# Performance work log

Hardware: AMD Instinct MI355X
Metric: run time of the kernel (lower is better)

Reference implementation:

```python
import jax, jax.numpy as jnp
import numpy as np

CODEC_RANGE = 1.0
COMMIT_WEIGHT = 0.1


def setup_inputs() -> dict:
    key = jax.random.key(0)
    ks = jax.random.split(key, 6)
    B, T, D, Dc, NQ, BINS = 8, 4096, 512, 256, 8, 1024
    return {
        "x": jax.random.normal(ks[0], (B, T, D), dtype=jnp.float32),
        "in_w": jax.random.normal(ks[1], (Dc, D), dtype=jnp.float32) * (1.0 / np.sqrt(D)),
        "in_b": jnp.zeros((Dc,), dtype=jnp.float32),
        "out_w": jax.random.normal(ks[2], (D, Dc), dtype=jnp.float32) * (1.0 / np.sqrt(Dc)),
        "out_b": jnp.zeros((D,), dtype=jnp.float32),
        "codebooks": jax.random.normal(ks[3], (NQ, BINS, Dc), dtype=jnp.float32),
    }


def reference(x, in_w, in_b, out_w, out_b, codebooks):
    # input projection + tanh range limiting
    h = jnp.tanh(x @ in_w.T + in_b) * CODEC_RANGE  # [B, T, Dc]

    def step(residual, codebook):
        # squared L2 distances: ||r||^2 - 2 r.e + ||e||^2  -> [B, T, bins]
        r2 = jnp.sum(residual * residual, axis=-1, keepdims=True)
        e2 = jnp.sum(codebook * codebook, axis=-1)  # [bins]
        dist = r2 - 2.0 * jnp.einsum("btd,nd->btn", residual, codebook) + e2
        idx = jnp.argmin(dist, axis=-1)  # [B, T]
        q = codebook[idx]  # gather -> [B, T, Dc]
        # commitment loss vs. detached quantized vectors
        commit = jnp.mean((jax.lax.stop_gradient(q) - residual) ** 2)
        return residual - q, (q, idx, commit)

    _, (qs, idxs, commits) = jax.lax.scan(step, h, codebooks)
    quantized = jnp.sum(qs, axis=0)  # [B, T, Dc]
    # straight-through estimator
    quantized = h + jax.lax.stop_gradient(quantized - h)
    out = quantized @ out_w.T + out_b  # [B, T, D]
    commit_loss = COMMIT_WEIGHT * jnp.sum(commits)
    return out, idxs, commit_loss
```

## Files before the change

kernel.cpp:

```cpp
#include <hip/hip_runtime.h>
#include <math.h>

#define DC 256
#define NBINS 1024
#define NQ 8
#define NTOK 32768
#define D_IN 512
#define DCH 32
#define TOK 64
#define STG_BLOCKS (NTOK / TOK)
#define MARGIN 5e-3f

typedef __attribute__((ext_vector_type(8))) short short8v;
typedef __attribute__((ext_vector_type(4))) float f32x4;

__device__ __forceinline__ unsigned short f2bf(float x) {
  unsigned u = __float_as_uint(x);
  return (unsigned short)((u + 0x7fffu + ((u >> 16) & 1u)) >> 16);
}
__device__ __forceinline__ float bf2f(unsigned short h) {
  return __uint_as_float(((unsigned)h) << 16);
}
__device__ __forceinline__ void store8s(unsigned short* dst, const unsigned short* v) {
  uint4 u;
  u.x = v[0] | ((unsigned)v[1] << 16); u.y = v[2] | ((unsigned)v[3] << 16);
  u.z = v[4] | ((unsigned)v[5] << 16); u.w = v[6] | ((unsigned)v[7] << 16);
  *reinterpret_cast<uint4*>(dst) = u;
}
__device__ __forceinline__ short8v load8s(const unsigned short* p) {
  return __builtin_bit_cast(short8v, *reinterpret_cast<const float4*>(p));
}

__device__ __forceinline__ float np_sumsq128(const float* a) {
#pragma clang fp contract(off)
  float r0 = a[0] * a[0], r1 = a[1] * a[1], r2 = a[2] * a[2], r3 = a[3] * a[3];
  float r4 = a[4] * a[4], r5 = a[5] * a[5], r6 = a[6] * a[6], r7 = a[7] * a[7];
  for (int i = 8; i < 128; i += 8) {
    r0 += a[i + 0] * a[i + 0]; r1 += a[i + 1] * a[i + 1];
    r2 += a[i + 2] * a[i + 2]; r3 += a[i + 3] * a[i + 3];
    r4 += a[i + 4] * a[i + 4]; r5 += a[i + 5] * a[i + 5];
    r6 += a[i + 6] * a[i + 6]; r7 += a[i + 7] * a[i + 7];
  }
  return ((r0 + r1) + (r2 + r3)) + ((r4 + r5) + (r6 + r7));
}
__device__ __forceinline__ float np_sumsq256(const float* a) {
#pragma clang fp contract(off)
  float lo = np_sumsq128(a);
  float hi = np_sumsq128(a + 128);
  return lo + hi;
}

__global__ void e2_np_kernel(const float* __restrict__ cb, float* __restrict__ e2) {
  int b = blockIdx.x * 256 + threadIdx.x;
  e2[b] = np_sumsq256(cb + (size_t)b * DC);
}

__global__ void presplit_kernel(const float* __restrict__ cb,
                                unsigned short* __restrict__ cb_h,
                                unsigned short* __restrict__ cb_l) {
  int id = blockIdx.x * 256 + threadIdx.x;
  int sk = id >> 10, bin = id & 1023;
  int s = sk >> 5, k8 = sk & 31;
  const float* src = cb + ((size_t)s * NBINS + bin) * DC + k8 * 8;
  unsigned short hh[8], ll[8];
#pragma unroll
  for (int j = 0; j < 8; ++j) {
    float x = src[j];
    unsigned short h = f2bf(x);
    hh[j] = h;
    ll[j] = f2bf(x - bf2f(h));
  }
  store8s(cb_h + (size_t)id * 8, hh);
  store8s(cb_l + (size_t)id * 8, ll);
}

__global__ __launch_bounds__(256) void in_proj_kernel(
    const float* __restrict__ x, const float* __restrict__ in_w,
    const float* __restrict__ in_b, float* __restrict__ res) {
  __shared__ __align__(16) float aT[DCH][68];
  __shared__ __align__(16) float bT[DCH][68];
  const int thr = threadIdx.x;
  const int tx = thr & 15, ty = thr >> 4;
  const int m0 = blockIdx.x * 64, n0 = blockIdx.y * 64;
  float acc[4][4] = {};
  float s1[4][4] = {};
  for (int kc = 0; kc < D_IN; kc += DCH) {
    if (kc == 384) {
#pragma unroll
      for (int i = 0; i < 4; ++i)
#pragma unroll
        for (int j = 0; j < 4; ++j) { s1[i][j] = acc[i][j]; acc[i][j] = 0.f; }
    }
    __syncthreads();
#pragma unroll
    for (int i = 0; i < 2; ++i) {
      int q = thr + 256 * i;
      int m = q >> 3, kk = (q & 7) << 2;
      float4 v = *reinterpret_cast<const float4*>(x + (size_t)(m0 + m) * D_IN + kc + kk);
      aT[kk + 0][m] = v.x; aT[kk + 1][m] = v.y; aT[kk + 2][m] = v.z; aT[kk + 3][m] = v.w;
      float4 w = *reinterpret_cast<const float4*>(in_w + (size_t)(n0 + m) * D_IN + kc + kk);
      bT[kk + 0][m] = w.x; bT[kk + 1][m] = w.y; bT[kk + 2][m] = w.z; bT[kk + 3][m] = w.w;
    }
    __syncthreads();
#pragma unroll 8
    for (int d = 0; d < DCH; ++d) {
      float4 a = *reinterpret_cast<const float4*>(&aT[d][ty * 4]);
      float4 b = *reinterpret_cast<const float4*>(&bT[d][tx * 4]);
      float av[4] = {a.x, a.y, a.z, a.w};
      float bv[4] = {b.x, b.y, b.z, b.w};
#pragma unroll
      for (int i = 0; i < 4; ++i)
#pragma unroll
        for (int j = 0; j < 4; ++j) acc[i][j] = fmaf(av[i], bv[j], acc[i][j]);
    }
  }
#pragma unroll
  for (int i = 0; i < 4; ++i) {
    int m = m0 + ty * 4 + i, n = n0 + tx * 4;
    float4 hv;
#pragma unroll
    for (int j = 0; j < 4; ++j) {
#pragma clang fp contract(off)
      float c = s1[i][j] + acc[i][j];
      float pre = c + in_b[n + j];
      ((float*)&hv)[j] = tanhf(pre);
    }
    *reinterpret_cast<float4*>(res + (size_t)m * DC + n) = hv;
  }
}

__global__ __launch_bounds__(256, 2) void score_kernel(
    const float* __restrict__ e2,
    const unsigned short* __restrict__ cb_h, const unsigned short* __restrict__ cb_l,
    const float* __restrict__ res, int* __restrict__ win_g, int* __restrict__ flag_g,
    int s) {
  __shared__ __align__(16) unsigned short a_hi[32 * TOK * 8];
  __shared__ __align__(16) unsigned short a_lo[32 * TOK * 8];
  __shared__ float m1s[4 * TOK], m2s[4 * TOK];
  __shared__ int   i1s[4 * TOK];

  const int thr = threadIdx.x;
  const int lane = thr & 63;
  const int w = thr >> 6;
  const int lg = lane >> 4;
  const int lc = lane & 15;
  const int m0 = blockIdx.x * TOK;
  const float* e2s = e2 + (size_t)s * NBINS;
  const unsigned short* bhp = cb_h + (size_t)s * (32 * 1024 * 8);
  const unsigned short* blp = cb_l + (size_t)s * (32 * 1024 * 8);

  {
    int row = thr >> 2, d0 = (thr & 3) << 6;
    const float* rrow = res + (size_t)(m0 + row) * DC + d0;
#pragma unroll
    for (int c = 0; c < 8; ++c) {
      float4 r0 = *reinterpret_cast<const float4*>(rrow + c * 8);
      float4 r1 = *reinterpret_cast<const float4*>(rrow + c * 8 + 4);
      float rv[8] = {r0.x, r0.y, r0.z, r0.w, r1.x, r1.y, r1.z, r1.w};
      unsigned short hh[8], ll[8];
#pragma unroll
      for (int j = 0; j < 8; ++j) {
        float xv = -2.0f * rv[j];
        unsigned short h = f2bf(xv);
        hh[j] = h; ll[j] = f2bf(xv - bf2f(h));
      }
      int k8 = (d0 >> 3) + c;
      store8s(a_hi + ((size_t)k8 * TOK + row) * 8, hh);
      store8s(a_lo + ((size_t)k8 * TOK + row) * 8, ll);
    }
  }
  m1s[thr] = 3.4028235e38f; m2s[thr] = 3.4028235e38f; i1s[thr] = 0;
  __syncthreads();

  for (int c = 0; c < 4; ++c) {
    const int bbase = w * 256 + c * 64;
    f32x4 acc[4][4];
#pragma unroll
    for (int nt = 0; nt < 4; ++nt) {
      float ev = e2s[bbase + nt * 16 + lc];
      f32x4 iv = {ev, ev, ev, ev};
#pragma unroll
      for (int rt = 0; rt < 4; ++rt) acc[rt][nt] = iv;
    }
#pragma unroll 2
    for (int kstep = 0; kstep < 8; ++kstep) {
      short8v ah[4], al[4];
#pragma unroll
      for (int rt = 0; rt < 4; ++rt) {
        int off = ((kstep * 4 + lg) * TOK + rt * 16 + lc) * 8;
        ah[rt] = load8s(a_hi + off);
        al[rt] = load8s(a_lo + off);
      }
      short8v bh[4], bl[4];
#pragma unroll
      for (int nt = 0; nt < 4; ++nt) {
        size_t boff = ((size_t)(kstep * 4 + lg) * 1024 + bbase + nt * 16 + lc) * 8;
        bh[nt] = load8s(bhp + boff);
        bl[nt] = load8s(blp + boff);
      }
#pragma unroll
      for (int nt = 0; nt < 4; ++nt)
#pragma unroll
        for (int rt = 0; rt < 4; ++rt)
          acc[rt][nt] = __builtin_amdgcn_mfma_f32_16x16x32_bf16(ah[rt], bh[nt], acc[rt][nt], 0, 0, 0);
#pragma unroll
      for (int nt = 0; nt < 4; ++nt)
#pragma unroll
        for (int rt = 0; rt < 4; ++rt)
          acc[rt][nt] = __builtin_amdgcn_mfma_f32_16x16x32_bf16(ah[rt], bl[nt], acc[rt][nt], 0, 0, 0);
#pragma unroll
      for (int nt = 0; nt < 4; ++nt)
#pragma unroll
        for (int rt = 0; rt < 4; ++rt)
          acc[rt][nt] = __builtin_amdgcn_mfma_f32_16x16x32_bf16(al[rt], bh[nt], acc[rt][nt], 0, 0, 0);
    }
#pragma unroll
    for (int rt = 0; rt < 4; ++rt)
#pragma unroll
      for (int reg = 0; reg < 4; ++reg) {
        float m1 = 3.4028235e38f, m2 = 3.4028235e38f; int i1 = 0;
#pragma unroll
        for (int nt = 0; nt < 4; ++nt) {
          float v = acc[rt][nt][reg];
          int b = bbase + nt * 16 + lc;
          if (v < m1) { m2 = m1; m1 = v; i1 = b; }
          else m2 = fminf(m2, v);
        }
#pragma unroll
        for (int msk = 1; msk < 16; msk <<= 1) {
          float om1 = __shfl_xor(m1, msk, 64);
          float om2 = __shfl_xor(m2, msk, 64);
          int   oi1 = __shfl_xor(i1, msk, 64);
          if (om1 < m1 || (om1 == m1 && oi1 < i1)) { m2 = fminf(m1, om2); m1 = om1; i1 = oi1; }
          else m2 = fminf(m2, om1);
        }
        if (lc == 0) {
          int sidx = w * TOK + rt * 16 + lg * 4 + reg;
          float pm1 = m1s[sidx], pm2 = m2s[sidx]; int pi1 = i1s[sidx];
          if (m1 < pm1 || (m1 == pm1 && i1 < pi1)) {
            m1s[sidx] = m1; m2s[sidx] = fminf(pm1, m2); i1s[sidx] = i1;
          } else {
            m2s[sidx] = fminf(pm2, m1);
          }
        }
      }
  }
  __syncthreads();
  if (thr < TOK) {
    float m1 = m1s[thr], m2 = m2s[thr]; int i1 = i1s[thr];
#pragma unroll
    for (int ww = 1; ww < 4; ++ww) {
      float om1 = m1s[ww * TOK + thr], om2 = m2s[ww * TOK + thr];
      int oi1 = i1s[ww * TOK + thr];
      if (om1 < m1 || (om1 == m1 && oi1 < i1)) { m2 = fminf(m1, om2); m1 = om1; i1 = oi1; }
      else m2 = fminf(m2, om1);
    }
    win_g[m0 + thr] = i1;
    flag_g[m0 + thr] = (m2 - m1 < MARGIN) ? 1 : 0;
  }
}

__global__ __launch_bounds__(256) void fix_kernel(
    const float* __restrict__ cb, const float* __restrict__ e2,
    const int* __restrict__ win_g, const int* __restrict__ flag_g,
    float* __restrict__ res, float* __restrict__ idx_f, double* __restrict__ partial,
    int s) {
  __shared__ int win_l[TOK], flag_l[TOK];
  __shared__ __align__(16) float rrow_s[256];
  __shared__ float redf[4];
  __shared__ int   redi[4];
  __shared__ double wsum[4];
  const int thr = threadIdx.x;
  const int lane = thr & 63;
  const int w = thr >> 6;
  const int m0 = blockIdx.x * TOK;
  const float* cbs = cb + (size_t)s * NBINS * DC;
  const float* e2s = e2 + (size_t)s * NBINS;
  double sqacc = 0.0;

  if (thr < TOK) { win_l[thr] = win_g[m0 + thr]; flag_l[thr] = flag_g[m0 + thr]; }
  __syncthreads();
  for (int row = 0; row < TOK; ++row) {
    if (!flag_l[row]) continue;
    if (thr < 64)
      reinterpret_cast<float4*>(rrow_s)[thr] =
          reinterpret_cast<const float4*>(res + (size_t)(m0 + row) * DC)[thr];
    __syncthreads();
    float r2 = np_sumsq256(rrow_s);
    float best = 3.4028235e38f; int bb = 0;
#pragma unroll
    for (int jj = 0; jj < 4; ++jj) {
      int b = thr * 4 + jj;
      const float4* e4 = reinterpret_cast<const float4*>(cbs + (size_t)b * DC);
      const float4* r4 = reinterpret_cast<const float4*>(rrow_s);
      float accv = 0.f;
      for (int q = 0; q < 64; ++q) {
        float4 ev = e4[q], rv = r4[q];
        accv = fmaf(rv.x, ev.x, accv);
        accv = fmaf(rv.y, ev.y, accv);
        accv = fmaf(rv.z, ev.z, accv);
        accv = fmaf(rv.w, ev.w, accv);
      }
      {
#pragma clang fp contract(off)
        float t = r2 - 2.0f * accv;
        float dist = t + e2s[b];
        if (dist < best) { best = dist; bb = b; }
      }
    }
#pragma unroll
    for (int msk = 1; msk < 64; msk <<= 1) {
      float ov = __shfl_xor(best, msk, 64);
      int   ob = __shfl_xor(bb, msk, 64);
      if (ov < best || (ov == best && ob < bb)) { best = ov; bb = ob; }
    }
    if (lane == 0) { redf[w] = best; redi[w] = bb; }
    __syncthreads();
    if (thr == 0) {
      float bs = redf[0]; int bfin = redi[0];
#pragma unroll
      for (int ww = 1; ww < 4; ++ww)
        if (redf[ww] < bs || (redf[ww] == bs && redi[ww] < bfin)) { bs = redf[ww]; bfin = redi[ww]; }
      win_l[row] = bfin;
    }
    __syncthreads();
  }
  {
    int row = thr >> 2, d0 = (thr & 3) << 6;
    int wbin = win_l[row];
    const float* erow = cbs + (size_t)wbin * DC + d0;
    float* rrow = res + (size_t)(m0 + row) * DC + d0;
#pragma unroll
    for (int c = 0; c < 8; ++c) {
      float4 r0 = *reinterpret_cast<const float4*>(rrow + c * 8);
      float4 r1 = *reinterpret_cast<const float4*>(rrow + c * 8 + 4);
      float4 e0 = *reinterpret_cast<const float4*>(erow + c * 8);
      float4 e1 = *reinterpret_cast<const float4*>(erow + c * 8 + 4);
      float nv[8] = {r0.x - e0.x, r0.y - e0.y, r0.z - e0.z, r0.w - e0.w,
                     r1.x - e1.x, r1.y - e1.y, r1.z - e1.z, r1.w - e1.w};
#pragma unroll
      for (int j = 0; j < 8; ++j) sqacc += (double)nv[j] * nv[j];
      *reinterpret_cast<float4*>(rrow + c * 8) = (float4){nv[0], nv[1], nv[2], nv[3]};
      *reinterpret_cast<float4*>(rrow + c * 8 + 4) = (float4){nv[4], nv[5], nv[6], nv[7]};
    }
    if (thr < TOK) idx_f[(size_t)s * NTOK + m0 + thr] = (float)win_l[thr];
  }
#pragma unroll
  for (int msk = 1; msk < 64; msk <<= 1) sqacc += __shfl_xor(sqacc, msk, 64);
  if (lane == 0) wsum[w] = sqacc;
  __syncthreads();
  if (thr == 0) {
    double t = 0.0;
#pragma unroll
    for (int ww = 0; ww < 4; ++ww) t += wsum[ww];
    partial[(size_t)s * STG_BLOCKS + blockIdx.x] = t;
  }
}

__global__ void finalize_kernel(const double* __restrict__ partial, float* __restrict__ out_last) {
  __shared__ double acc_s[64];
  int t = threadIdx.x;
  double a = 0.0;
  for (int i = 0; i < 64; ++i) a += partial[(size_t)t * 64 + i];
  acc_s[t] = a;
  __syncthreads();
  if (t == 0) {
    double tot = 0.0;
    for (int i = 0; i < 64; ++i) tot += acc_s[i];
    out_last[0] = (float)(0.1 * tot / 8388608.0);
  }
}

__global__ __launch_bounds__(256) void out_proj_kernel(
    const float* __restrict__ cb, const float* __restrict__ idx_f,
    const float* __restrict__ out_w, const float* __restrict__ out_b,
    float* __restrict__ out) {
  __shared__ __align__(16) float aT[DCH][68];
  __shared__ __align__(16) float bT[DCH][68];
  __shared__ int idx_l[NQ][64];
  const int thr = threadIdx.x;
  const int tx = thr & 15, ty = thr >> 4;
  const int m0 = blockIdx.x * 64, n0 = blockIdx.y * 64;
#pragma unroll
  for (int i = 0; i < 2; ++i) {
    int q = thr + 256 * i;
    int s = q >> 6, m = q & 63;
    idx_l[s][m] = (int)idx_f[(size_t)s * NTOK + m0 + m];
  }
  float acc[4][4] = {};
  for (int kc = 0; kc < DC; kc += DCH) {
    __syncthreads();
#pragma unroll
    for (int i = 0; i < 2; ++i) {
      int q = thr + 256 * i;
      int m = q >> 3, kk = (q & 7) << 2;
      float4 v = {0.f, 0.f, 0.f, 0.f};
#pragma unroll
      for (int s = 0; s < NQ; ++s) {
        const float4 e = *reinterpret_cast<const float4*>(
            cb + ((size_t)s * NBINS + idx_l[s][m]) * DC + kc + kk);
        v.x += e.x; v.y += e.y; v.z += e.z; v.w += e.w;
      }
      aT[kk + 0][m] = v.x; aT[kk + 1][m] = v.y; aT[kk + 2][m] = v.z; aT[kk + 3][m] = v.w;
      float4 wv = *reinterpret_cast<const float4*>(out_w + (size_t)(n0 + m) * DC + kc + kk);
      bT[kk + 0][m] = wv.x; bT[kk + 1][m] = wv.y; bT[kk + 2][m] = wv.z; bT[kk + 3][m] = wv.w;
    }
    __syncthreads();
#pragma unroll 8
    for (int d = 0; d < DCH; ++d) {
      float4 a = *reinterpret_cast<const float4*>(&aT[d][ty * 4]);
      float4 b = *reinterpret_cast<const float4*>(&bT[d][tx * 4]);
      float av[4] = {a.x, a.y, a.z, a.w};
      float bv[4] = {b.x, b.y, b.z, b.w};
#pragma unroll
      for (int i = 0; i < 4; ++i)
#pragma unroll
        for (int j = 0; j < 4; ++j) acc[i][j] = fmaf(av[i], bv[j], acc[i][j]);
    }
  }
#pragma unroll
  for (int i = 0; i < 4; ++i) {
    int m = m0 + ty * 4 + i, n = n0 + tx * 4;
    float4 o;
    o.x = acc[i][0] + out_b[n + 0];
    o.y = acc[i][1] + out_b[n + 1];
    o.z = acc[i][2] + out_b[n + 2];
    o.w = acc[i][3] + out_b[n + 3];
    *reinterpret_cast<float4*>(out + (size_t)m * D_IN + n) = o;
  }
}

extern "C" void kernel_launch(void* const* d_in, const int* in_sizes, int n_in,
                              void* d_out, int out_size, void* d_ws, size_t ws_size,
                              hipStream_t stream) {
  (void)in_sizes; (void)n_in; (void)out_size; (void)d_ws; (void)ws_size;
  const float* x     = (const float*)d_in[0];
  const float* in_w  = (const float*)d_in[1];
  const float* in_b  = (const float*)d_in[2];
  const float* out_w = (const float*)d_in[3];
  const float* out_b = (const float*)d_in[4];
  const float* cb    = (const float*)d_in[5];
  float* out = (float*)d_out;
  float* res    = out;
  float* e2     = out + 8388608;
  double* part  = (double*)(out + 8404992);
  unsigned short* cb_h = (unsigned short*)(out + 9000000);
  unsigned short* cb_l = (unsigned short*)(out + 10500000);
  int* win_g   = (int*)(out + 11600000);
  int* flag_g  = (int*)(out + 11700000);
  float* idx_f  = out + 16777216;
  float* c_out  = out + 17039360;

  hipLaunchKernelGGL(e2_np_kernel, dim3(32), dim3(256), 0, stream, cb, e2);
  hipLaunchKernelGGL(presplit_kernel, dim3(1024), dim3(256), 0, stream, cb, cb_h, cb_l);
  hipLaunchKernelGGL(in_proj_kernel, dim3(512, 4), dim3(256), 0, stream, x, in_w, in_b, res);
  for (int s = 0; s < NQ; ++s) {
    hipLaunchKernelGGL(score_kernel, dim3(STG_BLOCKS), dim3(256), 0, stream,
                       e2, cb_h, cb_l, res, win_g, flag_g, s);
    hipLaunchKernelGGL(fix_kernel, dim3(STG_BLOCKS), dim3(256), 0, stream,
                       cb, e2, win_g, flag_g, res, idx_f, part, s);
  }
  hipLaunchKernelGGL(finalize_kernel, dim3(1), dim3(64), 0, stream, part, c_out);
  hipLaunchKernelGGL(out_proj_kernel, dim3(512, 8), dim3(256), 0, stream, cb, idx_f, out_w, out_b, out);
}
```

Before: 1.562 ms.

## Move output projection to bf16x3 MFMA with full-N tiles per block

The output projection now runs on MFMA bf16 instructions, using a hi/lo split (three products) to keep near-fp32 accuracy, in place of scalar FMA tiling. Each block handles 32 tokens across all 512 output columns. The summed codebook vectors are gathered once per token into shared memory, which removes the repeated gathers the old 64x64 tiling did for every N tile. out_w is read directly from global memory and split into bf16 halves inside the loop, which adds conversion ALU work and uncoalesced weight loads. Stores are scalar and strided.

```diff
diff --git a/kernel.cpp b/kernel.cpp
--- a/kernel.cpp
+++ b/kernel.cpp
@@ -26,6 +26,12 @@
   u.x = v[0] | ((unsigned)v[1] << 16); u.y = v[2] | ((unsigned)v[3] << 16);
   u.z = v[4] | ((unsigned)v[5] << 16); u.w = v[6] | ((unsigned)v[7] << 16);
   *reinterpret_cast<uint4*>(dst) = u;
+}
+__device__ __forceinline__ short8v pack8s(const unsigned short* v) {
+  uint4 u;
+  u.x = v[0] | ((unsigned)v[1] << 16); u.y = v[2] | ((unsigned)v[3] << 16);
+  u.z = v[4] | ((unsigned)v[5] << 16); u.w = v[6] | ((unsigned)v[7] << 16);
+  return __builtin_bit_cast(short8v, u);
 }
 __device__ __forceinline__ short8v load8s(const unsigned short* p) {
   return __builtin_bit_cast(short8v, *reinterpret_cast<const float4*>(p));
@@ -375,59 +381,95 @@
     const float* __restrict__ cb, const float* __restrict__ idx_f,
     const float* __restrict__ out_w, const float* __restrict__ out_b,
     float* __restrict__ out) {
-  __shared__ __align__(16) float aT[DCH][68];
-  __shared__ __align__(16) float bT[DCH][68];
-  __shared__ int idx_l[NQ][64];
+  __shared__ __align__(16) unsigned short a_hi[32 * 32 * 8];
+  __shared__ __align__(16) unsigned short a_lo[32 * 32 * 8];
   const int thr = threadIdx.x;
-  const int tx = thr & 15, ty = thr >> 4;
-  const int m0 = blockIdx.x * 64, n0 = blockIdx.y * 64;
-#pragma unroll
-  for (int i = 0; i < 2; ++i) {
-    int q = thr + 256 * i;
-    int s = q >> 6, m = q & 63;
-    idx_l[s][m] = (int)idx_f[(size_t)s * NTOK + m0 + m];
-  }
-  float acc[4][4] = {};
-  for (int kc = 0; kc < DC; kc += DCH) {
-    __syncthreads();
-#pragma unroll
-    for (int i = 0; i < 2; ++i) {
-      int q = thr + 256 * i;
-      int m = q >> 3, kk = (q & 7) << 2;
-      float4 v = {0.f, 0.f, 0.f, 0.f};
+  const int lane = thr & 63;
+  const int w = thr >> 6;
+  const int lg = lane >> 4;
+  const int lc = lane & 15;
+  const int m0 = blockIdx.x * 32;
+
+  {
+    int row = thr >> 3, d0 = (thr & 7) << 5;
+    int m = m0 + row;
+    int idxs[NQ];
+#pragma unroll
+    for (int s = 0; s < NQ; ++s) idxs[s] = (int)idx_f[(size_t)s * NTOK + m];
+#pragma unroll
+    for (int c = 0; c < 4; ++c) {
+      int d = d0 + c * 8;
+      float q[8] = {0.f, 0.f, 0.f, 0.f, 0.f, 0.f, 0.f, 0.f};
 #pragma unroll
       for (int s = 0; s < NQ; ++s) {
-        const float4 e = *reinterpret_cast<const float4*>(
-            cb + ((size_t)s * NBINS + idx_l[s][m]) * DC + kc + kk);
-        v.x += e.x; v.y += e.y; v.z += e.z; v.w += e.w;
-      }
-      aT[kk + 0][m] = v.x; aT[kk + 1][m] = v.y; aT[kk + 2][m] = v.z; aT[kk + 3][m] = v.w;
-      float4 wv = *reinterpret_cast<const float4*>(out_w + (size_t)(n0 + m) * DC + kc + kk);
-      bT[kk + 0][m] = wv.x; bT[kk + 1][m] = wv.y; bT[kk + 2][m] = wv.z; bT[kk + 3][m] = wv.w;
-    }
-    __syncthreads();
-#pragma unroll 8
-    for (int d = 0; d < DCH; ++d) {
-      float4 a = *reinterpret_cast<const float4*>(&aT[d][ty * 4]);
-      float4 b = *reinterpret_cast<const float4*>(&bT[d][tx * 4]);
-      float av[4] = {a.x, a.y, a.z, a.w};
-      float bv[4] = {b.x, b.y, b.z, b.w};
-#pragma unroll
-      for (int i = 0; i < 4; ++i)
-#pragma unroll
-        for (int j = 0; j < 4; ++j) acc[i][j] = fmaf(av[i], bv[j], acc[i][j]);
-    }
-  }
-#pragma unroll
-  for (int i = 0; i < 4; ++i) {
-    int m = m0 + ty * 4 + i, n = n0 + tx * 4;
-    float4 o;
-    o.x = acc[i][0] + out_b[n + 0];
-    o.y = acc[i][1] + out_b[n + 1];
-    o.z = acc[i][2] + out_b[n + 2];
-    o.w = acc[i][3] + out_b[n + 3];
-    *reinterpret_cast<float4*>(out + (size_t)m * D_IN + n) = o;
-  }
+        const float4* e4 = reinterpret_cast<const float4*>(
+            cb + ((size_t)s * NBINS + idxs[s]) * DC + d);
+        float4 e0 = e4[0], e1 = e4[1];
+        q[0] += e0.x; q[1] += e0.y; q[2] += e0.z; q[3] += e0.w;
+        q[4] += e1.x; q[5] += e1.y; q[6] += e1.z; q[7] += e1.w;
+      }
+      unsigned short hh[8], ll[8];
+#pragma unroll
+      for (int j = 0; j < 8; ++j) {
+        unsigned short h = f2bf(q[j]);
+        hh[j] = h; ll[j] = f2bf(q[j] - bf2f(h));
+      }
+      int k8 = d >> 3;
+      store8s(a_hi + ((size_t)k8 * 32 + row) * 8, hh);
+      store8s(a_lo + ((size_t)k8 * 32 + row) * 8, ll);
+    }
+  }
+  __syncthreads();
+
+  f32x4 acc[2][8];
+#pragma unroll
+  for (int nt = 0; nt < 8; ++nt) {
+    float bv = out_b[w * 128 + nt * 16 + lc];
+    f32x4 iv = {bv, bv, bv, bv};
+    acc[0][nt] = iv; acc[1][nt] = iv;
+  }
+#pragma unroll 2
+  for (int kstep = 0; kstep < 8; ++kstep) {
+    short8v ah[2], al[2];
+#pragma unroll
+    for (int rt = 0; rt < 2; ++rt) {
+      int off = ((kstep * 4 + lg) * 32 + rt * 16 + lc) * 8;
+      ah[rt] = load8s(a_hi + off);
+      al[rt] = load8s(a_lo + off);
+    }
+#pragma unroll
+    for (int nt = 0; nt < 8; ++nt) {
+      int n = w * 128 + nt * 16 + lc;
+      const float* wp = out_w + (size_t)n * DC + (kstep * 4 + lg) * 8;
+      float4 w0 = *reinterpret_cast<const float4*>(wp);
+      float4 w1 = *reinterpret_cast<const float4*>(wp + 4);
+      float wv[8] = {w0.x, w0.y, w0.z, w0.w, w1.x, w1.y, w1.z, w1.w};
+      unsigned short bhh[8], bll[8];
+#pragma unroll
+      for (int j = 0; j < 8; ++j) {
+        unsigned short h = f2bf(wv[j]);
+        bhh[j] = h; bll[j] = f2bf(wv[j] - bf2f(h));
+      }
+      short8v bh = pack8s(bhh), bl = pack8s(bll);
+      acc[0][nt] = __builtin_amdgcn_mfma_f32_16x16x32_bf16(ah[0], bh, acc[0][nt], 0, 0, 0);
+      acc[1][nt] = __builtin_amdgcn_mfma_f32_16x16x32_bf16(ah[1], bh, acc[1][nt], 0, 0, 0);
+      acc[0][nt] = __builtin_amdgcn_mfma_f32_16x16x32_bf16(ah[0], bl, acc[0][nt], 0, 0, 0);
+      acc[1][nt] = __builtin_amdgcn_mfma_f32_16x16x32_bf16(ah[1], bl, acc[1][nt], 0, 0, 0);
+      acc[0][nt] = __builtin_amdgcn_mfma_f32_16x16x32_bf16(al[0], bh, acc[0][nt], 0, 0, 0);
+      acc[1][nt] = __builtin_amdgcn_mfma_f32_16x16x32_bf16(al[1], bh, acc[1][nt], 0, 0, 0);
+    }
+  }
+#pragma unroll
+  for (int rt = 0; rt < 2; ++rt)
+#pragma unroll
+    for (int nt = 0; nt < 8; ++nt) {
+      int n = w * 128 + nt * 16 + lc;
+#pragma unroll
+      for (int reg = 0; reg < 4; ++reg) {
+        int m = m0 + rt * 16 + lg * 4 + reg;
+        out[(size_t)m * D_IN + n] = acc[rt][nt][reg];
+      }
+    }
 }
 
 extern "C" void kernel_launch(void* const* d_in, const int* in_sizes, int n_in,
@@ -461,5 +503,5 @@
                        cb, e2, win_g, flag_g, res, idx_f, part, s);
   }
   hipLaunchKernelGGL(finalize_kernel, dim3(1), dim3(64), 0, stream, part, c_out);
-  hipLaunchKernelGGL(out_proj_kernel, dim3(512, 8), dim3(256), 0, stream, cb, idx_f, out_w, out_b, out);
-}
+  hipLaunchKernelGGL(out_proj_kernel, dim3(1024), dim3(256), 0, stream, cb, idx_f, out_w, out_b, out);
+}
```

Measured after the change: 1.491 ms. 1.05x faster.
